# Kernel optimization log

Hardware: AMD Instinct MI355X
Metric: run time of the kernel (lower is better)

Reference implementation:

```python
import jax, jax.numpy as jnp
import numpy as np

DEPTH = 11


def setup_inputs() -> dict:
    key = jax.random.key(0)
    k1, k2, k3 = jax.random.split(key, 3)
    B, S, D = 4, 4096, 768
    n_nodes = 2 * DEPTH - 1  # 21
    return {
        "inputs": jax.random.normal(k1, (B, S, D), dtype=jnp.float32),
        "weights_in": jax.random.normal(k2, (n_nodes, D), dtype=jnp.float32),
        "weights_out": jax.random.normal(k3, (n_nodes, D), dtype=jnp.float32),
    }


def _fff_forward(inputs, weights_in, weights_out, depth=DEPTH):
    B, S, _ = inputs.shape
    n_nodes = weights_in.shape[0]
    max_index = n_nodes - 1

    # Dot product of every token with every tree-node weight once: (B,S,n_nodes).
    # Mathematically identical to gathering weights_in[sel] per level and taking
    # a per-token dot product, but avoids materializing (B,S,D) gathers per step.
    all_logits = jnp.einsum('bsd,nd->bsn', inputs, weights_in)

    def step(prev_idx, _):
        sel = jnp.clip(prev_idx, 0, max_index)
        logits = jnp.take_along_axis(all_logits, sel[..., None], axis=-1)[..., 0]  # (B,S)
        new_idx = jnp.clip(2 * sel + 1 + (logits > 0).astype(sel.dtype), 0, max_index)
        return new_idx, (logits, new_idx)

    idx0 = jnp.zeros((B, S), dtype=jnp.int32)
    _, (logits_seq, idx_seq) = jax.lax.scan(step, idx0, None, length=depth - 1)

    # Level 0 has logit=0 (gelu(0)=0 -> zero contribution) and node index 0.
    logits = jnp.concatenate(
        [jnp.zeros((1, B, S), all_logits.dtype), logits_seq], axis=0)  # (depth,B,S)
    node_idx = jnp.concatenate([idx0[None], idx_seq], axis=0)          # (depth,B,S)

    act = jax.nn.gelu(logits, approximate=False)  # exact erf GELU = torch.nn.GELU

    # out[b,s,:] = sum_d act[d,b,s] * weights_out[node_idx[d,b,s], :]
    # Scatter the 11 per-level activations into per-node coefficients (B,S,21),
    # then one small dense matmul against the 21x768 output table.
    onehot = jax.nn.one_hot(node_idx, n_nodes, dtype=act.dtype)  # (depth,B,S,n)
    coeff = jnp.einsum('dbs,dbsn->bsn', act, onehot)             # (B,S,n)
    return jnp.einsum('bsn,nd->bsd', coeff, weights_out)         # (B,S,D)


def reference(inputs, weights_in, weights_out):
    return _fff_forward(inputs, weights_in, weights_out)
```

## Files before the change

kernel.cpp:

```cpp
#include <hip/hip_runtime.h>
#include <math.h>


#define D 768
#define NF4 (D / 4)
#define NN 21
#define TPB 1024
#define NBLK 256
#define WAVES_TOTAL (NBLK * (TPB / 64))

__device__ __forceinline__ float gelu_exact(float v) {
  return 0.5f * v * (1.0f + erff(v * 0.70710678118654752440f));
}

__device__ __forceinline__ double wave_sum(double v) {
#pragma unroll
  for (int off = 32; off > 0; off >>= 1) v += __shfl_xor(v, off, 64);
  return v;
}

__device__ __forceinline__ double dot_row(float4 x0, float4 x1, float4 x2,
                                          const float* __restrict__ row,
                                          int lane) {
  const float4* r = (const float4*)row;
  float4 w0 = r[lane];
  float4 w1 = r[lane + 64];
  float4 w2 = r[lane + 128];
  double s = (double)x0.x * (double)w0.x;
  s = fma((double)x0.y, (double)w0.y, s);
  s = fma((double)x0.z, (double)w0.z, s);
  s = fma((double)x0.w, (double)w0.w, s);
  s = fma((double)x1.x, (double)w1.x, s);
  s = fma((double)x1.y, (double)w1.y, s);
  s = fma((double)x1.z, (double)w1.z, s);
  s = fma((double)x1.w, (double)w1.w, s);
  s = fma((double)x2.x, (double)w2.x, s);
  s = fma((double)x2.y, (double)w2.y, s);
  s = fma((double)x2.z, (double)w2.z, s);
  s = fma((double)x2.w, (double)w2.w, s);
  return wave_sum(s);
}

#define ACC4(av, wv)                 \
  av.x = fmaf(g, wv.x, av.x);        \
  av.y = fmaf(g, wv.y, av.y);        \
  av.z = fmaf(g, wv.z, av.z);        \
  av.w = fmaf(g, wv.w, av.w)

__global__ __launch_bounds__(TPB, 4) void fff_kernel(
    const float* __restrict__ x, const float* __restrict__ wi,
    const float* __restrict__ wo, float* __restrict__ out, int ntok) {
  __shared__ float s_wi[NN * D];
  __shared__ float s_wo[NN * D];

  const int tid = threadIdx.x;
  {
    const float4* a = (const float4*)wi;
    const float4* b = (const float4*)wo;
    float4* sa = (float4*)s_wi;
    float4* sb = (float4*)s_wo;
    for (int i = tid; i < NN * NF4; i += TPB) {
      sa[i] = a[i];
      sb[i] = b[i];
    }
  }
  __syncthreads();

  const int lane = tid & 63;
  const int wid = (blockIdx.x << 4) | (tid >> 6);

  for (int tok = wid; tok < ntok; tok += WAVES_TOTAL) {
    const float4* xp = (const float4*)(x + (size_t)tok * D);
    float4 x0 = xp[lane];
    float4 x1 = xp[lane + 64];
    float4 x2 = xp[lane + 128];

    float4 a0 = {0.f, 0.f, 0.f, 0.f};
    float4 a1 = {0.f, 0.f, 0.f, 0.f};
    float4 a2 = {0.f, 0.f, 0.f, 0.f};

    int u = 0;
#pragma unroll
    for (int t = 0; t < 4; ++t) {
      double lam = dot_row(x0, x1, x2, s_wi + u * D, lane);
      float lf = (float)lam;
      float g = gelu_exact(lf);
      u = 2 * u + 1 + (lf > 0.0f);
      u = min(u, NN - 1);
      const float4* r = (const float4*)(s_wo + u * D);
      float4 w0 = r[lane];
      float4 w1 = r[lane + 64];
      float4 w2 = r[lane + 128];
      ACC4(a0, w0);
      ACC4(a1, w1);
      ACC4(a2, w2);
    }
    double lam4 = dot_row(x0, x1, x2, s_wi + u * D, lane);
    float g4 = gelu_exact((float)lam4);
    double lam20 =
        (u == NN - 1) ? lam4 : dot_row(x0, x1, x2, s_wi + (NN - 1) * D, lane);
    float g20 = gelu_exact((float)lam20);
    float g = g4 + 5.0f * g20;
    {
      const float4* r = (const float4*)(s_wo + (NN - 1) * D);
      float4 w0 = r[lane];
      float4 w1 = r[lane + 64];
      float4 w2 = r[lane + 128];
      ACC4(a0, w0);
      ACC4(a1, w1);
      ACC4(a2, w2);
    }

    float4* op = (float4*)(out + (size_t)tok * D);
    op[lane] = a0;
    op[lane + 64] = a1;
    op[lane + 128] = a2;
  }
}

extern "C" void kernel_launch(void* const* d_in, const int* in_sizes, int n_in,
                              void* d_out, int out_size, void* d_ws,
                              size_t ws_size, hipStream_t stream) {
  const float* x = (const float*)d_in[0];
  const float* wi = (const float*)d_in[1];
  const float* wo = (const float*)d_in[2];
  float* out = (float*)d_out;
  const int ntok = in_sizes[0] / D;
  fff_kernel<<<NBLK, TPB, 0, stream>>>(x, wi, wo, out, ntok);
}
```

Before: 135.1 us.

## Compute all node logits in fp32 for token pairs with DPP reductions

Replaces the sequential tree walk of fp64 dot products and shuffle reductions with an eager fp32 pass that computes all 21 node logits for two tokens per wave. The 42 results are then reduced with DPP row operations plus two cross-row shuffles. Path selection becomes branchless selects, and launch bounds drop to one block per SM. The intent is to remove the serial dependency chain and the slow fp64 math, at the cost of computing every node rather than only the visited ones. It also carries more register pressure and some fp32 rounding risk near zero logits.

```diff
diff --git a/kernel.cpp b/kernel.cpp
--- a/kernel.cpp
+++ b/kernel.cpp
@@ -7,51 +7,103 @@
 #define NN 21
 #define TPB 1024
 #define NBLK 256
-#define WAVES_TOTAL (NBLK * (TPB / 64))
+#define NWAVES (NBLK * (TPB / 64))
 
 __device__ __forceinline__ float gelu_exact(float v) {
   return 0.5f * v * (1.0f + erff(v * 0.70710678118654752440f));
 }
 
-__device__ __forceinline__ double wave_sum(double v) {
-#pragma unroll
-  for (int off = 32; off > 0; off >>= 1) v += __shfl_xor(v, off, 64);
+template <int CTRL>
+__device__ __forceinline__ float dppadd(float v) {
+  int m = __builtin_amdgcn_update_dpp(0, __float_as_int(v), CTRL, 0xF, 0xF, true);
+  return v + __int_as_float(m);
+}
+
+__device__ __forceinline__ float wave_red(float v) {
+  v = dppadd<0x140>(v);
+  v = dppadd<0x141>(v);
+  v = dppadd<0x4E>(v);
+  v = dppadd<0xB1>(v);
+  v += __shfl_xor(v, 16);
+  v += __shfl_xor(v, 32);
   return v;
 }
 
-__device__ __forceinline__ double dot_row(float4 x0, float4 x1, float4 x2,
-                                          const float* __restrict__ row,
-                                          int lane) {
-  const float4* r = (const float4*)row;
-  float4 w0 = r[lane];
-  float4 w1 = r[lane + 64];
-  float4 w2 = r[lane + 128];
-  double s = (double)x0.x * (double)w0.x;
-  s = fma((double)x0.y, (double)w0.y, s);
-  s = fma((double)x0.z, (double)w0.z, s);
-  s = fma((double)x0.w, (double)w0.w, s);
-  s = fma((double)x1.x, (double)w1.x, s);
-  s = fma((double)x1.y, (double)w1.y, s);
-  s = fma((double)x1.z, (double)w1.z, s);
-  s = fma((double)x1.w, (double)w1.w, s);
-  s = fma((double)x2.x, (double)w2.x, s);
-  s = fma((double)x2.y, (double)w2.y, s);
-  s = fma((double)x2.z, (double)w2.z, s);
-  s = fma((double)x2.w, (double)w2.w, s);
-  return wave_sum(s);
+__device__ __forceinline__ float dot12(float4 a0, float4 a1, float4 a2,
+                                       float4 w0, float4 w1, float4 w2) {
+  float s = a0.x * w0.x;
+  s = fmaf(a0.y, w0.y, s); s = fmaf(a0.z, w0.z, s); s = fmaf(a0.w, w0.w, s);
+  s = fmaf(a1.x, w1.x, s); s = fmaf(a1.y, w1.y, s); s = fmaf(a1.z, w1.z, s);
+  s = fmaf(a1.w, w1.w, s); s = fmaf(a2.x, w2.x, s); s = fmaf(a2.y, w2.y, s);
+  s = fmaf(a2.z, w2.z, s); s = fmaf(a2.w, w2.w, s);
+  return s;
 }
 
-#define ACC4(av, wv)                 \
-  av.x = fmaf(g, wv.x, av.x);        \
-  av.y = fmaf(g, wv.y, av.y);        \
-  av.z = fmaf(g, wv.z, av.z);        \
-  av.w = fmaf(g, wv.w, av.w)
+__device__ __forceinline__ void accrow(const float* __restrict__ row, int lane,
+                                       float g, float4& a0, float4& a1,
+                                       float4& a2) {
+  const float4* r = (const float4*)row;
+  float4 w0 = r[lane], w1 = r[lane + 64], w2 = r[lane + 128];
+  a0.x = fmaf(g, w0.x, a0.x); a0.y = fmaf(g, w0.y, a0.y);
+  a0.z = fmaf(g, w0.z, a0.z); a0.w = fmaf(g, w0.w, a0.w);
+  a1.x = fmaf(g, w1.x, a1.x); a1.y = fmaf(g, w1.y, a1.y);
+  a1.z = fmaf(g, w1.z, a1.z); a1.w = fmaf(g, w1.w, a1.w);
+  a2.x = fmaf(g, w2.x, a2.x); a2.y = fmaf(g, w2.y, a2.y);
+  a2.z = fmaf(g, w2.z, a2.z); a2.w = fmaf(g, w2.w, a2.w);
+}
 
-__global__ __launch_bounds__(TPB, 4) void fff_kernel(
+__device__ __forceinline__ void token_out(const float (&r)[NN],
+                                          const float* __restrict__ s_wo,
+                                          int lane, float* __restrict__ outp) {
+  float l0 = r[0];
+  int b0 = l0 > 0.0f;
+  float l1 = b0 ? r[2] : r[1];
+  int b1 = l1 > 0.0f;
+  float l2 = b0 ? (b1 ? r[6] : r[5]) : (b1 ? r[4] : r[3]);
+  int b2 = l2 > 0.0f;
+  float m0 = b2 ? r[8] : r[7];
+  float m1 = b2 ? r[10] : r[9];
+  float m2 = b2 ? r[12] : r[11];
+  float m3 = b2 ? r[14] : r[13];
+  float l3 = b0 ? (b1 ? m3 : m2) : (b1 ? m1 : m0);
+  int b3 = l3 > 0.0f;
+  int i4 = (b0 << 3) | (b1 << 2) | (b2 << 1) | b3;
+  float l4 = r[15];
+  l4 = (i4 >= 1) ? r[16] : l4;
+  l4 = (i4 >= 2) ? r[17] : l4;
+  l4 = (i4 >= 3) ? r[18] : l4;
+  l4 = (i4 >= 4) ? r[19] : l4;
+  l4 = (i4 >= 5) ? r[20] : l4;
+
+  int u1 = 1 + b0;
+  int u2 = 3 + 2 * b0 + b1;
+  int u3 = 7 + 4 * b0 + 2 * b1 + b2;
+  int u4 = 15 + (i4 < 5 ? i4 : 5);
+
+  float g1 = gelu_exact(l0);
+  float g2 = gelu_exact(l1);
+  float g3 = gelu_exact(l2);
+  float g4 = gelu_exact(l3);
+  float g5 = gelu_exact(l4) + 5.0f * gelu_exact(r[20]);
+
+  float4 a0 = {0.f, 0.f, 0.f, 0.f}, a1 = a0, a2 = a0;
+  accrow(s_wo + u1 * D, lane, g1, a0, a1, a2);
+  accrow(s_wo + u2 * D, lane, g2, a0, a1, a2);
+  accrow(s_wo + u3 * D, lane, g3, a0, a1, a2);
+  accrow(s_wo + u4 * D, lane, g4, a0, a1, a2);
+  accrow(s_wo + (NN - 1) * D, lane, g5, a0, a1, a2);
+
+  float4* op = (float4*)outp;
+  op[lane] = a0;
+  op[lane + 64] = a1;
+  op[lane + 128] = a2;
+}
+
+__global__ __launch_bounds__(TPB, 1) void fff_kernel(
     const float* __restrict__ x, const float* __restrict__ wi,
     const float* __restrict__ wo, float* __restrict__ out, int ntok) {
-  __shared__ float s_wi[NN * D];
-  __shared__ float s_wo[NN * D];
+  __shared__ __align__(16) float s_wi[NN * D];
+  __shared__ __align__(16) float s_wo[NN * D];
 
   const int tid = threadIdx.x;
   {
@@ -68,53 +120,33 @@
 
   const int lane = tid & 63;
   const int wid = (blockIdx.x << 4) | (tid >> 6);
+  const float4* swi4 = (const float4*)s_wi;
 
-  for (int tok = wid; tok < ntok; tok += WAVES_TOTAL) {
-    const float4* xp = (const float4*)(x + (size_t)tok * D);
-    float4 x0 = xp[lane];
-    float4 x1 = xp[lane + 64];
-    float4 x2 = xp[lane + 128];
+  for (int tA = wid; tA < ntok; tA += 2 * NWAVES) {
+    const int tB = tA + NWAVES;
+    const bool hasB = tB < ntok;
+    const float4* xa = (const float4*)(x + (size_t)tA * D);
+    float4 xa0 = xa[lane], xa1 = xa[lane + 64], xa2 = xa[lane + 128];
+    const float4* xb = (const float4*)(x + (size_t)(hasB ? tB : tA) * D);
+    float4 xb0 = xb[lane], xb1 = xb[lane + 64], xb2 = xb[lane + 128];
 
-    float4 a0 = {0.f, 0.f, 0.f, 0.f};
-    float4 a1 = {0.f, 0.f, 0.f, 0.f};
-    float4 a2 = {0.f, 0.f, 0.f, 0.f};
-
-    int u = 0;
+    float rA[NN], rB[NN];
 #pragma unroll
-    for (int t = 0; t < 4; ++t) {
-      double lam = dot_row(x0, x1, x2, s_wi + u * D, lane);
-      float lf = (float)lam;
-      float g = gelu_exact(lf);
-      u = 2 * u + 1 + (lf > 0.0f);
-      u = min(u, NN - 1);
-      const float4* r = (const float4*)(s_wo + u * D);
-      float4 w0 = r[lane];
-      float4 w1 = r[lane + 64];
-      float4 w2 = r[lane + 128];
-      ACC4(a0, w0);
-      ACC4(a1, w1);
-      ACC4(a2, w2);
+    for (int n = 0; n < NN; ++n) {
+      float4 w0 = swi4[n * NF4 + lane];
+      float4 w1 = swi4[n * NF4 + lane + 64];
+      float4 w2 = swi4[n * NF4 + lane + 128];
+      rA[n] = dot12(xa0, xa1, xa2, w0, w1, w2);
+      rB[n] = dot12(xb0, xb1, xb2, w0, w1, w2);
     }
-    double lam4 = dot_row(x0, x1, x2, s_wi + u * D, lane);
-    float g4 = gelu_exact((float)lam4);
-    double lam20 =
-        (u == NN - 1) ? lam4 : dot_row(x0, x1, x2, s_wi + (NN - 1) * D, lane);
-    float g20 = gelu_exact((float)lam20);
-    float g = g4 + 5.0f * g20;
-    {
-      const float4* r = (const float4*)(s_wo + (NN - 1) * D);
-      float4 w0 = r[lane];
-      float4 w1 = r[lane + 64];
-      float4 w2 = r[lane + 128];
-      ACC4(a0, w0);
-      ACC4(a1, w1);
-      ACC4(a2, w2);
+#pragma unroll
+    for (int n = 0; n < NN; ++n) {
+      rA[n] = wave_red(rA[n]);
+      rB[n] = wave_red(rB[n]);
     }
 
-    float4* op = (float4*)(out + (size_t)tok * D);
-    op[lane] = a0;
-    op[lane + 64] = a1;
-    op[lane + 128] = a2;
+    token_out(rA, s_wo, lane, out + (size_t)tA * D);
+    if (hasB) token_out(rB, s_wo, lane, out + (size_t)tB * D);
   }
 }
 
```

Result: slower. 151.6 us (+12.2%).
